# Kernel tuning notes

Measured on AMD Instinct MI355X. Metric: run time of the kernel, lower is better.

## Reference

```python
import jax, jax.numpy as jnp
import numpy as np

EMBED_DIM = 1024
NUM_HEADS = 16
HEAD_DIM = EMBED_DIM // NUM_HEADS
SCALE = HEAD_DIM ** -0.5


def setup_inputs() -> dict:
    key = jax.random.key(0)
    ks = jax.random.split(key, 5)
    B, N, C = 4, 2048, EMBED_DIM
    s = C ** -0.5
    return {
        "x": jax.random.normal(ks[0], (B, N, C), dtype=jnp.float32),
        "w_qkv": jax.random.normal(ks[1], (C, 3 * C), dtype=jnp.float32) * s,
        "b_qkv": jnp.zeros((3 * C,), dtype=jnp.float32),
        "w_proj": jax.random.normal(ks[2], (C, C), dtype=jnp.float32) * s,
        "b_proj": jnp.zeros((C,), dtype=jnp.float32),
    }


def reference(x, w_qkv, b_qkv, w_proj, b_proj):
    B, N, C = x.shape
    H, D = NUM_HEADS, HEAD_DIM
    qkv = x @ w_qkv + b_qkv                      # (B, N, 3C)
    qkv = qkv.reshape(B, N, 3, H, D)
    qkv = jnp.transpose(qkv, (2, 0, 3, 1, 4))    # (3, B, H, N, D)
    q, k, v = qkv[0], qkv[1], qkv[2]
    attn = jnp.einsum('bhnd,bhmd->bhnm', q, k) * SCALE
    attn = jax.nn.softmax(attn, axis=-1)
    out = jnp.einsum('bhnm,bhmd->bhnd', attn, v)  # (B, H, N, D)
    out = jnp.transpose(out, (0, 2, 1, 3)).reshape(B, N, C)
    return out @ w_proj + b_proj
```

## Files before the change

kernel.cpp:

```cpp
#include <hip/hip_runtime.h>

typedef __attribute__((ext_vector_type(8))) short short8v;
typedef __attribute__((ext_vector_type(4))) short short4v;
typedef __attribute__((ext_vector_type(4))) float float4v;
typedef __attribute__((ext_vector_type(4))) unsigned short ushort4v;
typedef __attribute__((ext_vector_type(8))) unsigned short ushort8v;

#define GLOBAL_AS __attribute__((address_space(1)))
#define LDS_AS __attribute__((address_space(3)))

__device__ __forceinline__ void async_cp16(const void* g, void* l) {
  __builtin_amdgcn_global_load_lds((const GLOBAL_AS void*)g, (LDS_AS void*)l, 16, 0, 0);
}

__device__ __forceinline__ unsigned short f2bf(float f) {
  unsigned u = __float_as_uint(f);
  u += 0x7fffu + ((u >> 16) & 1u);
  return (unsigned short)(u >> 16);
}

#if defined(__HIP_DEVICE_COMPILE__)
#if __has_builtin(__builtin_amdgcn_mfma_f32_16x16x16bf16_1k)
#define MFMA_PV(a, b, c) __builtin_amdgcn_mfma_f32_16x16x16bf16_1k(a, b, c, 0, 0, 0)
#elif __has_builtin(__builtin_amdgcn_mfma_f32_16x16x16_bf16_1k)
#define MFMA_PV(a, b, c) __builtin_amdgcn_mfma_f32_16x16x16_bf16_1k(a, b, c, 0, 0, 0)
#elif __has_builtin(__builtin_amdgcn_mfma_f32_16x16x16_bf16)
#define MFMA_PV(a, b, c) __builtin_amdgcn_mfma_f32_16x16x16_bf16(a, b, c, 0, 0, 0)
#else
#error "no 16x16x16 bf16 mfma builtin on device"
#endif
#if __has_builtin(__builtin_amdgcn_exp2f)
#define EXP2F(x) __builtin_amdgcn_exp2f(x)
#else
#define EXP2F(x) exp2f(x)
#endif
#else
#define MFMA_PV(a, b, c) (c)
#define EXP2F(x) exp2f(x)
#endif

#if defined(__HIP_DEVICE_COMPILE__) && __has_builtin(__builtin_amdgcn_cvt_pk_bf16_f32)
typedef __attribute__((ext_vector_type(2))) __bf16 bf16x2v;
__device__ __forceinline__ unsigned pk_bf16(float a, float b) {
  bf16x2v r = __builtin_amdgcn_cvt_pk_bf16_f32(a, b);
  return __builtin_bit_cast(unsigned, r);
}
#else
__device__ __forceinline__ unsigned pk_bf16(float a, float b) {
  return (unsigned)f2bf(a) | ((unsigned)f2bf(b) << 16);
}
#endif

#define MFMA_QK(a, b, c) __builtin_amdgcn_mfma_f32_16x16x32_bf16(a, b, c, 0, 0, 0)


__global__ __launch_bounds__(256) void cvt_f32_bf16(const float* __restrict__ src,
                                                    unsigned short* __restrict__ dst) {
  int i = blockIdx.x * 256 + threadIdx.x;
  float4 v = ((const float4*)src)[i];
  ushort4v o;
  o.x = f2bf(v.x); o.y = f2bf(v.y); o.z = f2bf(v.z); o.w = f2bf(v.w);
  ((ushort4v*)dst)[i] = o;
}

__global__ __launch_bounds__(256) void transpose_w(const float* __restrict__ src,
                                                   unsigned short* __restrict__ dst,
                                                   int K, int N) {
  __shared__ float tile[64][65];
  int k0 = blockIdx.x * 64, n0 = blockIdx.y * 64;
  int t = threadIdx.x;
  int tc = t & 15, tr = t >> 4;
#pragma unroll
  for (int p = 0; p < 4; p++) {
    int r = tr + p * 16;
    float4 v = *(const float4*)(src + (size_t)(k0 + r) * N + n0 + tc * 4);
    tile[r][tc * 4 + 0] = v.x; tile[r][tc * 4 + 1] = v.y;
    tile[r][tc * 4 + 2] = v.z; tile[r][tc * 4 + 3] = v.w;
  }
  __syncthreads();
#pragma unroll
  for (int p = 0; p < 4; p++) {
    int rn = tr + p * 16;
    ushort4v o;
    o.x = f2bf(tile[tc * 4 + 0][rn]);
    o.y = f2bf(tile[tc * 4 + 1][rn]);
    o.z = f2bf(tile[tc * 4 + 2][rn]);
    o.w = f2bf(tile[tc * 4 + 3][rn]);
    *(ushort4v*)(dst + (size_t)(n0 + rn) * K + k0 + tc * 4) = o;
  }
}


__global__ __launch_bounds__(256) void gemm_qkv(const unsigned short* __restrict__ A,
                                                const unsigned short* __restrict__ BT,
                                                const float* __restrict__ bias,
                                                unsigned short* __restrict__ Qo,
                                                unsigned short* __restrict__ Ko,
                                                unsigned short* __restrict__ VTo) {
  __shared__ unsigned short As[128 * 32];
  __shared__ unsigned short Bs[128 * 32];
  int tid = threadIdx.x;
  int lane = tid & 63, w = tid >> 6, g = lane >> 4, c = lane & 15;
  int m0 = blockIdx.x * 128, n0 = blockIdx.y * 128;
  int wm = (w & 1) * 64, wn = (w >> 1) * 64;
  float4v acc[4][4] = {};

  for (int k0 = 0; k0 < 1024; k0 += 32) {
    __syncthreads();
#pragma unroll
    for (int p = 0; p < 2; p++) {
      int idx = p * 256 + tid;
      int row = idx >> 2, c8 = (idx & 3) * 8;
      async_cp16(A + (size_t)(m0 + row) * 1024 + k0 + c8, &As[idx * 8]);
      async_cp16(BT + (size_t)(n0 + row) * 1024 + k0 + c8, &Bs[idx * 8]);
    }
    __syncthreads();
    short8v af[4], bf[4];
#pragma unroll
    for (int i = 0; i < 4; i++)
      af[i] = *(const short8v*)(&As[(wm + i * 16 + c) * 32 + g * 8]);
#pragma unroll
    for (int j = 0; j < 4; j++)
      bf[j] = *(const short8v*)(&Bs[(wn + j * 16 + c) * 32 + g * 8]);
#pragma unroll
    for (int i = 0; i < 4; i++)
#pragma unroll
      for (int j = 0; j < 4; j++)
        acc[i][j] = MFMA_QK(af[i], bf[j], acc[i][j]);
  }

  int which = n0 >> 10;
#pragma unroll
  for (int j = 0; j < 4; j++) {
    int ng = n0 + wn + j * 16 + c;
    float bv = bias[ng];
    int h = (ng & 1023) >> 6, d = ng & 63;
#pragma unroll
    for (int i = 0; i < 4; i++) {
#pragma unroll
      for (int r = 0; r < 4; r++) {
        int mg = m0 + wm + i * 16 + g * 4 + r;
        int b = mg >> 11, n = mg & 2047;
        float v = acc[i][j][r] + bv;
        if (which == 0)
          Qo[((size_t)(b * 16 + h) * 2048 + n) * 64 + d] = f2bf(v * 0.18033688011112042f);
        else if (which == 1)
          Ko[((size_t)(b * 16 + h) * 2048 + n) * 64 + d] = f2bf(v);
        else
          VTo[((size_t)(b * 16 + h) * 64 + d) * 2048 + n] = f2bf(v);
      }
    }
  }
}


#define NTOK 2048
#define VTS 132

__global__ __launch_bounds__(256) void attn_kernel(const unsigned short* __restrict__ Qg,
                                                   const unsigned short* __restrict__ Kg,
                                                   const unsigned short* __restrict__ VTg,
                                                   unsigned short* __restrict__ Og) {
  __shared__ unsigned short Ks[128 * 64];
  __shared__ unsigned short VTsm[64 * VTS];

  int tid = threadIdx.x;
  int lane = tid & 63, w = tid >> 6, g = lane >> 4, c = lane & 15;
  int id = blockIdx.x;
  int xcd = id & 7, within = id >> 3;
  int bh = xcd * 8 + (within >> 4);
  int q0 = (within & 15) * 128;

  const unsigned short* Qb = Qg + (size_t)bh * NTOK * 64;
  const unsigned short* Kb = Kg + (size_t)bh * NTOK * 64;
  const unsigned short* VTb = VTg + (size_t)bh * 64 * NTOK;

  short8v qf[2][2];
#pragma unroll
  for (int nt = 0; nt < 2; nt++)
#pragma unroll
    for (int kk = 0; kk < 2; kk++)
      qf[nt][kk] = *(const short8v*)(Qb + (size_t)(q0 + w * 32 + nt * 16 + c) * 64 +
                                     kk * 32 + g * 8);

  short4v ones;
  ones.x = (short)0x3F80; ones.y = (short)0x3F80;
  ones.z = (short)0x3F80; ones.w = (short)0x3F80;

  float4v lacc[2] = {};
  float4v o[2][4] = {};

  for (int kt = 0; kt < NTOK; kt += 128) {
    __syncthreads();
#pragma unroll
    for (int p = 0; p < 4; p++) {
      int idx = p * 256 + tid;
      int row = idx >> 3, ch = idx & 7;
      async_cp16(Kb + (size_t)(kt + row) * 64 + ((ch ^ (row & 7)) * 8), &Ks[idx * 8]);
    }
    ushort8v vv[4];
    int vds[4], vcs[4];
#pragma unroll
    for (int p = 0; p < 4; p++) {
      int idx = p * 256 + tid;
      int d = idx >> 4, c8 = (idx & 15) * 8;
      vv[p] = *(const ushort8v*)(VTb + (size_t)d * NTOK + kt + c8);
      vds[p] = d; vcs[p] = c8;
    }
#pragma unroll
    for (int p = 0; p < 4; p++) {
      ushort4v lo = __builtin_shufflevector(vv[p], vv[p], 0, 1, 2, 3);
      ushort4v hi = __builtin_shufflevector(vv[p], vv[p], 4, 5, 6, 7);
      *(ushort4v*)(&VTsm[vds[p] * VTS + vcs[p]]) = lo;
      *(ushort4v*)(&VTsm[vds[p] * VTS + vcs[p] + 4]) = hi;
    }
    __syncthreads();

#pragma unroll
    for (int half = 0; half < 2; half++) {
      float4v st[4][2] = {};
#pragma unroll
      for (int mth = 0; mth < 4; mth++) {
        int mt = half * 4 + mth;
        int row = mt * 16 + c;
        short8v kf[2];
#pragma unroll
        for (int kk = 0; kk < 2; kk++) {
          int ch = (kk * 4 + g) ^ (row & 7);
          kf[kk] = *(const short8v*)(&Ks[row * 64 + ch * 8]);
        }
#pragma unroll
        for (int nt = 0; nt < 2; nt++)
#pragma unroll
          for (int kk = 0; kk < 2; kk++)
            st[mth][nt] = MFMA_QK(kf[kk], qf[nt][kk], st[mth][nt]);
      }

#pragma unroll
      for (int mth = 0; mth < 4; mth++) {
        int kk8 = half * 4 + mth;
        short4v pa[2];
#pragma unroll
        for (int nt = 0; nt < 2; nt++) {
          float4v p4 = st[mth][nt];
          p4.x = EXP2F(p4.x); p4.y = EXP2F(p4.y);
          p4.z = EXP2F(p4.z); p4.w = EXP2F(p4.w);
          union { unsigned u[2]; short4v s; } cv;
          cv.u[0] = pk_bf16(p4.x, p4.y);
          cv.u[1] = pk_bf16(p4.z, p4.w);
          pa[nt] = cv.s;
        }
#pragma unroll
        for (int nt_o = 0; nt_o < 4; nt_o++) {
          short4v vb = *(const short4v*)(&VTsm[(nt_o * 16 + c) * VTS + kk8 * 16 + g * 4]);
#pragma unroll
          for (int mt_o = 0; mt_o < 2; mt_o++)
            o[mt_o][nt_o] = MFMA_PV(pa[mt_o], vb, o[mt_o][nt_o]);
        }
#pragma unroll
        for (int mt_o = 0; mt_o < 2; mt_o++)
          lacc[mt_o] = MFMA_PV(pa[mt_o], ones, lacc[mt_o]);
      }
    }
  }

  int b = bh >> 4, h = bh & 15;
#pragma unroll
  for (int mt_o = 0; mt_o < 2; mt_o++) {
    float4v li;
#pragma unroll
    for (int r = 0; r < 4; r++) li[r] = 1.0f / lacc[mt_o][r];
#pragma unroll
    for (int nt_o = 0; nt_o < 4; nt_o++) {
      float4v v = o[mt_o][nt_o] * li;
      int col = h * 64 + nt_o * 16 + c;
      int rowbase = b * NTOK + q0 + w * 32 + mt_o * 16 + g * 4;
#pragma unroll
      for (int r = 0; r < 4; r++)
        Og[(size_t)(rowbase + r) * 1024 + col] = f2bf(v[r]);
    }
  }
}

__global__ __launch_bounds__(256) void gemm_proj(const unsigned short* __restrict__ A,
                                                 const unsigned short* __restrict__ BT,
                                                 const float* __restrict__ bias,
                                                 float* __restrict__ out) {
  __shared__ unsigned short As[128 * 32];
  __shared__ unsigned short Bs[128 * 32];
  int tid = threadIdx.x;
  int lane = tid & 63, w = tid >> 6, g = lane >> 4, c = lane & 15;
  int m0 = blockIdx.x * 128, n0 = blockIdx.y * 128;
  int wm = (w & 1) * 64, wn = (w >> 1) * 64;
  float4v acc[4][4] = {};

  for (int k0 = 0; k0 < 1024; k0 += 32) {
    __syncthreads();
#pragma unroll
    for (int p = 0; p < 2; p++) {
      int idx = p * 256 + tid;
      int row = idx >> 2, c8 = (idx & 3) * 8;
      async_cp16(A + (size_t)(m0 + row) * 1024 + k0 + c8, &As[idx * 8]);
      async_cp16(BT + (size_t)(n0 + row) * 1024 + k0 + c8, &Bs[idx * 8]);
    }
    __syncthreads();
    short8v af[4], bf[4];
#pragma unroll
    for (int i = 0; i < 4; i++)
      af[i] = *(const short8v*)(&As[(wm + i * 16 + c) * 32 + g * 8]);
#pragma unroll
    for (int j = 0; j < 4; j++)
      bf[j] = *(const short8v*)(&Bs[(wn + j * 16 + c) * 32 + g * 8]);
#pragma unroll
    for (int i = 0; i < 4; i++)
#pragma unroll
      for (int j = 0; j < 4; j++)
        acc[i][j] = MFMA_QK(af[i], bf[j], acc[i][j]);
  }

#pragma unroll
  for (int j = 0; j < 4; j++) {
    int ng = n0 + wn + j * 16 + c;
    float bv = bias[ng];
#pragma unroll
    for (int i = 0; i < 4; i++) {
#pragma unroll
      for (int r = 0; r < 4; r++) {
        int mg = m0 + wm + i * 16 + g * 4 + r;
        out[(size_t)mg * 1024 + ng] = acc[i][j][r] + bv;
      }
    }
  }
}


extern "C" void kernel_launch(void* const* d_in, const int* in_sizes, int n_in,
                              void* d_out, int out_size, void* d_ws, size_t ws_size,
                              hipStream_t stream) {
  (void)in_sizes; (void)n_in; (void)out_size; (void)ws_size;
  const float* x = (const float*)d_in[0];
  const float* w_qkv = (const float*)d_in[1];
  const float* b_qkv = (const float*)d_in[2];
  const float* w_proj = (const float*)d_in[3];
  const float* b_proj = (const float*)d_in[4];
  float* out = (float*)d_out;

  unsigned short* x_bf = (unsigned short*)d_ws;
  unsigned short* wqkvT = x_bf + (size_t)8192 * 1024;
  unsigned short* wprojT = wqkvT + (size_t)3072 * 1024;
  unsigned short* qws = wprojT + (size_t)1024 * 1024;
  unsigned short* kws = qws + (size_t)8388608;
  unsigned short* vtws = kws + (size_t)8388608;
  unsigned short* aws = vtws + (size_t)8388608;

  cvt_f32_bf16<<<8192, 256, 0, stream>>>(x, x_bf);
  transpose_w<<<dim3(16, 48), 256, 0, stream>>>(w_qkv, wqkvT, 1024, 3072);
  transpose_w<<<dim3(16, 16), 256, 0, stream>>>(w_proj, wprojT, 1024, 1024);
  gemm_qkv<<<dim3(64, 24), 256, 0, stream>>>(x_bf, wqkvT, b_qkv, qws, kws, vtws);
  attn_kernel<<<1024, 256, 0, stream>>>(qws, kws, vtws, aws);
  gemm_proj<<<dim3(64, 8), 256, 0, stream>>>(aws, wprojT, b_proj, out);
}
```

Before: 308.7 us.

## Double-buffer K/V tiles with async LDS loads and swizzled V layout

Shrinks the key tile from 128 to 64 and adds two LDS buffers for K and V. The next tile is now loaded with async global-to-LDS copies while the current one is being computed, so only one barrier is needed per iteration. V^T is also loaded with async copies into an XOR-swizzled layout instead of padded register-staged stores, and launch bounds now request four blocks per CU. This is meant to hide global load latency and remove the VGPR round trip for V, at the cost of twice as many loop iterations and barriers.

```diff
diff --git a/kernel.cpp b/kernel.cpp
--- a/kernel.cpp
+++ b/kernel.cpp
@@ -155,17 +155,18 @@
 
 
 #define NTOK 2048
-#define VTS 132
-
-__global__ __launch_bounds__(256) void attn_kernel(const unsigned short* __restrict__ Qg,
-                                                   const unsigned short* __restrict__ Kg,
-                                                   const unsigned short* __restrict__ VTg,
-                                                   unsigned short* __restrict__ Og) {
-  __shared__ unsigned short Ks[128 * 64];
-  __shared__ unsigned short VTsm[64 * VTS];
+#define BK 64
+
+__global__ __launch_bounds__(256, 4) void attn_kernel(const unsigned short* __restrict__ Qg,
+                                                      const unsigned short* __restrict__ Kg,
+                                                      const unsigned short* __restrict__ VTg,
+                                                      unsigned short* __restrict__ Og) {
+  __shared__ unsigned short Ks[2][BK * 64];
+  __shared__ unsigned short VTs[2][64 * BK];
 
   int tid = threadIdx.x;
   int lane = tid & 63, w = tid >> 6, g = lane >> 4, c = lane & 15;
+  int gh = g >> 1, g1 = g & 1;
   int id = blockIdx.x;
   int xcd = id & 7, within = id >> 3;
   int bh = xcd * 8 + (within >> 4);
@@ -190,44 +191,46 @@
   float4v lacc[2] = {};
   float4v o[2][4] = {};
 
-  for (int kt = 0; kt < NTOK; kt += 128) {
-    __syncthreads();
-#pragma unroll
-    for (int p = 0; p < 4; p++) {
-      int idx = p * 256 + tid;
-      int row = idx >> 3, ch = idx & 7;
-      async_cp16(Kb + (size_t)(kt + row) * 64 + ((ch ^ (row & 7)) * 8), &Ks[idx * 8]);
-    }
-    ushort8v vv[4];
-    int vds[4], vcs[4];
-#pragma unroll
-    for (int p = 0; p < 4; p++) {
-      int idx = p * 256 + tid;
-      int d = idx >> 4, c8 = (idx & 15) * 8;
-      vv[p] = *(const ushort8v*)(VTb + (size_t)d * NTOK + kt + c8);
-      vds[p] = d; vcs[p] = c8;
-    }
-#pragma unroll
-    for (int p = 0; p < 4; p++) {
-      ushort4v lo = __builtin_shufflevector(vv[p], vv[p], 0, 1, 2, 3);
-      ushort4v hi = __builtin_shufflevector(vv[p], vv[p], 4, 5, 6, 7);
-      *(ushort4v*)(&VTsm[vds[p] * VTS + vcs[p]]) = lo;
-      *(ushort4v*)(&VTsm[vds[p] * VTS + vcs[p] + 4]) = hi;
-    }
-    __syncthreads();
+#pragma unroll
+  for (int p = 0; p < 2; p++) {
+    int idx = p * 256 + tid;
+    int row = idx >> 3, ch = idx & 7;
+    async_cp16(Kb + (size_t)row * 64 + ((ch ^ (row & 7)) * 8), &Ks[0][idx * 8]);
+    async_cp16(VTb + (size_t)row * NTOK + ((ch ^ (row & 7)) * 8), &VTs[0][idx * 8]);
+  }
+
+  for (int it = 0; it < NTOK / BK; it++) {
+    int pb = it & 1;
+    __syncthreads();
+
+    if (it + 1 < NTOK / BK) {
+      int kt = (it + 1) * BK;
+#pragma unroll
+      for (int p = 0; p < 2; p++) {
+        int idx = p * 256 + tid;
+        int row = idx >> 3, ch = idx & 7;
+        async_cp16(Kb + (size_t)(kt + row) * 64 + ((ch ^ (row & 7)) * 8),
+                   &Ks[1 - pb][idx * 8]);
+        async_cp16(VTb + (size_t)row * NTOK + kt + ((ch ^ (row & 7)) * 8),
+                   &VTs[1 - pb][idx * 8]);
+      }
+    }
+
+    const unsigned short* Kp = &Ks[pb][0];
+    const unsigned short* Vp = &VTs[pb][0];
 
 #pragma unroll
     for (int half = 0; half < 2; half++) {
-      float4v st[4][2] = {};
-#pragma unroll
-      for (int mth = 0; mth < 4; mth++) {
-        int mt = half * 4 + mth;
+      float4v st[2][2] = {};
+#pragma unroll
+      for (int mth = 0; mth < 2; mth++) {
+        int mt = half * 2 + mth;
         int row = mt * 16 + c;
         short8v kf[2];
 #pragma unroll
         for (int kk = 0; kk < 2; kk++) {
           int ch = (kk * 4 + g) ^ (row & 7);
-          kf[kk] = *(const short8v*)(&Ks[row * 64 + ch * 8]);
+          kf[kk] = *(const short8v*)(Kp + row * 64 + ch * 8);
         }
 #pragma unroll
         for (int nt = 0; nt < 2; nt++)
@@ -237,8 +240,8 @@
       }
 
 #pragma unroll
-      for (int mth = 0; mth < 4; mth++) {
-        int kk8 = half * 4 + mth;
+      for (int mth = 0; mth < 2; mth++) {
+        int kk8 = half * 2 + mth;
         short4v pa[2];
 #pragma unroll
         for (int nt = 0; nt < 2; nt++) {
@@ -252,7 +255,9 @@
         }
 #pragma unroll
         for (int nt_o = 0; nt_o < 4; nt_o++) {
-          short4v vb = *(const short4v*)(&VTsm[(nt_o * 16 + c) * VTS + kk8 * 16 + g * 4]);
+          int d = nt_o * 16 + c;
+          int pc = (kk8 * 2 + gh) ^ (d & 7);
+          short4v vb = *(const short4v*)(Vp + d * BK + pc * 8 + g1 * 4);
 #pragma unroll
           for (int mt_o = 0; mt_o < 2; mt_o++)
             o[mt_o][nt_o] = MFMA_PV(pa[mt_o], vb, o[mt_o][nt_o]);
```

After: 304.8 us. About the same (-1.2%).
